# Performance work log

Hardware: AMD Instinct MI355X
Metric: run time of the kernel (lower is better)

Reference implementation:

```python
import jax, jax.numpy as jnp
import numpy as np

HIDDEN = 2048
HEADS = 16
HEAD_DIM = HIDDEN // HEADS  # 128
SCALE = 1.0 / float(np.sqrt(HEAD_DIM))
B, S = 2, 2048


def setup_inputs() -> dict:
    key = jax.random.key(0)
    ks = jax.random.split(key, 5)
    return {
        "x": jax.random.normal(ks[0], (B, S, HIDDEN), dtype=jnp.float32),
        "q_w": jax.random.normal(ks[1], (HIDDEN, HIDDEN), dtype=jnp.float32) * (HIDDEN ** -0.5),
        "k_w": jax.random.normal(ks[2], (HEAD_DIM, HIDDEN), dtype=jnp.float32) * (HIDDEN ** -0.5),
        "v_w": jax.random.normal(ks[3], (HEAD_DIM, HIDDEN), dtype=jnp.float32) * (HIDDEN ** -0.5),
        "o_w": jax.random.normal(ks[4], (HIDDEN, HIDDEN), dtype=jnp.float32) * (HIDDEN ** -0.5),
    }


def reference(x, q_w, k_w, v_w, o_w):
    b, s, _ = x.shape
    # torch F.linear: x @ W^T with W [out, in]
    q = (x @ q_w.T).reshape(b, s, HEADS, HEAD_DIM).transpose(0, 2, 1, 3)  # [B,H,S,D]
    k = x @ k_w.T  # [B,S,D] single shared KV head
    v = x @ v_w.T  # [B,S,D]
    # scores: [B,H,S,S] -- explicit O(S^2) materialization as in the source
    scores = jnp.einsum('bhqd,bkd->bhqk', q, k) * SCALE
    # softmax in float32 then cast back (matches dtype=torch.float32 then type_as)
    attn = jax.nn.softmax(scores.astype(jnp.float32), axis=-1).astype(q.dtype)
    out = jnp.einsum('bhqk,bkd->bhqd', attn, v)  # [B,H,S,D]
    out = out.transpose(0, 2, 1, 3).reshape(b, s, HIDDEN)
    return out @ o_w.T
```

## Files before the change

### kernel.cpp

```cpp
#include <hip/hip_runtime.h>
#include <stdint.h>

#define HID 2048
#define DHEAD 128
#define SEQL 2048
#define C2 0.1275187981510609f
#define MOFF 8.0f

typedef __attribute__((ext_vector_type(4))) float f32x4;
typedef __attribute__((ext_vector_type(8))) short s16x8;

__device__ __forceinline__ unsigned short bf16_rne(float f) {
  union { float f; unsigned u; } v; v.f = f;
  return (unsigned short)((v.u + 0x7FFFu + ((v.u >> 16) & 1u)) >> 16);
}

__device__ __forceinline__ void gload_lds16(const void* g, void* l) {
  __builtin_amdgcn_global_load_lds(
      (__attribute__((address_space(1))) unsigned int*)(void*)g,
      (__attribute__((address_space(3))) unsigned int*)l, 16, 0, 0);
}

__device__ __forceinline__ void cvt8(const float* __restrict__ in,
                                     unsigned short* __restrict__ out, int k) {
  const f32x4* p = (const f32x4*)in;
  f32x4 a = p[2 * k], b = p[2 * k + 1];
  union { s16x8 v; unsigned short s[8]; } o;
  o.s[0] = bf16_rne(a[0]); o.s[1] = bf16_rne(a[1]);
  o.s[2] = bf16_rne(a[2]); o.s[3] = bf16_rne(a[3]);
  o.s[4] = bf16_rne(b[0]); o.s[5] = bf16_rne(b[1]);
  o.s[6] = bf16_rne(b[2]); o.s[7] = bf16_rne(b[3]);
  ((s16x8*)out)[k] = o.v;
}

__global__ __launch_bounds__(256) void cvt_bf16_k(const float* __restrict__ in,
                                                  unsigned short* __restrict__ out,
                                                  int n8) {
  int i = blockIdx.x * 256 + threadIdx.x;
  if (i >= n8) return;
  cvt8(in, out, i);
}

__global__ __launch_bounds__(256) void cvt4_k(
    const float* __restrict__ s0, unsigned short* __restrict__ d0, int n0,
    const float* __restrict__ s1, unsigned short* __restrict__ d1, int n1,
    const float* __restrict__ s2, unsigned short* __restrict__ d2, int n2,
    const float* __restrict__ s3, unsigned short* __restrict__ d3, int n3) {
  int i = blockIdx.x * 256 + threadIdx.x;
  if (i < n0) { cvt8(s0, d0, i); return; }
  i -= n0;
  if (i < n1) { cvt8(s1, d1, i); return; }
  i -= n1;
  if (i < n2) { cvt8(s2, d2, i); return; }
  i -= n2;
  if (i < n3) { cvt8(s3, d3, i); return; }
}

template <int LOG2SLOTS>
__device__ __forceinline__ void stage_tile(const unsigned short* __restrict__ src,
                                           int ld, char* smem, int t) {
  int w = t >> 6;
#pragma unroll
  for (int i = 0; i < 4; ++i) {
    int c = i * 256 + t;
    int row = c >> LOG2SLOTS;
    int slot = c & ((1 << LOG2SLOTS) - 1);
    gload_lds16(src + row * ld + ((slot ^ (row & 7)) << 3),
                smem + (i * 256 + w * 64) * 16);
  }
}

template <int MODE>
__global__ __launch_bounds__(256, 2) void gemm_bt(
    const unsigned short* __restrict__ A, const unsigned short* __restrict__ Bw,
    void* __restrict__ Cout, int M, int N, int K, unsigned short* __restrict__ Vt) {
  __shared__ char As[2][16384];
  __shared__ char Bs[2][16384];
  int t = threadIdx.x;
  int lane = t & 63, w = t >> 6;
  int wm = w >> 1, wn = w & 1;
  int l15 = lane & 15, l4 = lane >> 4;

  int gdx = gridDim.x;
  int nwg = gdx * gridDim.y;
  int bid = blockIdx.y * gdx + blockIdx.x;
  int q8 = nwg >> 3;
  int swz = (bid & 7) * q8 + (bid >> 3);
  int tm = (swz / gdx) * 128, tn = (swz % gdx) * 128;

  f32x4 acc[4][4] = {};

  stage_tile<3>(A + tm * K, K, As[0], t);
  stage_tile<3>(Bw + tn * K, K, Bs[0], t);
  asm volatile("s_waitcnt vmcnt(0)" ::: "memory");
  __builtin_amdgcn_s_barrier();

  int nk = K >> 6;
  for (int ki = 0; ki < nk; ++ki) {
    int cur = ki & 1;
    if (ki + 1 < nk) {
      stage_tile<3>(A + tm * K + (ki + 1) * 64, K, As[cur ^ 1], t);
      stage_tile<3>(Bw + tn * K + (ki + 1) * 64, K, Bs[cur ^ 1], t);
    }
    const char* as = As[cur];
    const char* bs = Bs[cur];
    s16x8 af[4][2], bfr[4][2];
#pragma unroll
    for (int m = 0; m < 4; ++m)
#pragma unroll
      for (int kk = 0; kk < 2; ++kk) {
        int row = wm * 64 + m * 16 + l15;
        af[m][kk] = *(const s16x8*)(as + row * 128 + (((kk * 4 + l4) ^ (row & 7)) << 4));
      }
#pragma unroll
    for (int n = 0; n < 4; ++n)
#pragma unroll
      for (int kk = 0; kk < 2; ++kk) {
        int row = wn * 64 + n * 16 + l15;
        bfr[n][kk] = *(const s16x8*)(bs + row * 128 + (((kk * 4 + l4) ^ (row & 7)) << 4));
      }
#pragma unroll
    for (int m = 0; m < 4; ++m)
#pragma unroll
      for (int n = 0; n < 4; ++n)
#pragma unroll
        for (int kk = 0; kk < 2; ++kk)
          acc[m][n] = __builtin_amdgcn_mfma_f32_16x16x32_bf16(af[m][kk], bfr[n][kk],
                                                              acc[m][n], 0, 0, 0);
    asm volatile("s_waitcnt vmcnt(0) lgkmcnt(0)" ::: "memory");
    __builtin_amdgcn_sched_barrier(0);
    __builtin_amdgcn_s_barrier();
  }

#pragma unroll
  for (int m = 0; m < 4; ++m)
#pragma unroll
    for (int n = 0; n < 4; ++n) {
      int col = tn + wn * 64 + n * 16 + l15;
#pragma unroll
      for (int j = 0; j < 4; ++j) {
        int row = tm + wm * 64 + m * 16 + l4 * 4 + j;
        float v = acc[m][n][j];
        if (MODE == 0) {
          ((unsigned short*)Cout)[row * N + col] = bf16_rne(v);
        } else if (MODE == 1) {
          ((float*)Cout)[row * N + col] = v;
        } else {
          if (col < 128) {
            ((unsigned short*)Cout)[row * 128 + col] = bf16_rne(v);
          } else {
            int d = col - 128, bb = row >> 11, s = row & 2047;
            Vt[((bb * 128 + d) << 11) + s] = bf16_rne(v);
          }
        }
      }
    }
}

__global__ __launch_bounds__(256, 2) void attn_k(
    const unsigned short* __restrict__ Q, const unsigned short* __restrict__ Kb,
    const unsigned short* __restrict__ Vt, unsigned short* __restrict__ AO) {
  __shared__ char Ks[2][16384];
  __shared__ char Vs[2][16384];
  int t = threadIdx.x;
  int lane = t & 63, w = t >> 6;
  int l15 = lane & 15, l4 = lane >> 4;
  int qt = blockIdx.x, bh = blockIdx.y;
  int b = bh >> 4, h = bh & 15;
  int qg = b * SEQL + qt * 128 + w * 32;

  s16x8 qf[2][4];
#pragma unroll
  for (int m = 0; m < 2; ++m)
#pragma unroll
    for (int kc = 0; kc < 4; ++kc)
      qf[m][kc] = *(const s16x8*)(Q + (qg + m * 16 + l15) * HID + h * DHEAD + kc * 32 + l4 * 8);

  union { s16x8 v; unsigned short s[8]; } one_;
#pragma unroll
  for (int i = 0; i < 8; ++i) one_.s[i] = 0x3F80;
  const s16x8 ones = one_.v;

  f32x4 oacc[2][9] = {};

  {
#pragma unroll
    for (int i = 0; i < 4; ++i) {
      int c = i * 256 + t, row = c >> 4, slot = c & 15;
      gload_lds16(Kb + (b * SEQL + row) * DHEAD + ((slot ^ (row & 7)) << 3),
                  Ks[0] + (i * 256 + w * 64) * 16);
    }
#pragma unroll
    for (int i = 0; i < 4; ++i) {
      int c = i * 256 + t, row = c >> 3, slot = c & 7;
      gload_lds16(Vt + (b * DHEAD + row) * SEQL + ((slot ^ (row & 7)) << 3),
                  Vs[0] + (i * 256 + w * 64) * 16);
    }
  }
  asm volatile("s_waitcnt vmcnt(0)" ::: "memory");
  __builtin_amdgcn_s_barrier();

  for (int kv = 0; kv < SEQL; kv += 64) {
    int cur = (kv >> 6) & 1;
    if (kv + 64 < SEQL) {
#pragma unroll
      for (int i = 0; i < 4; ++i) {
        int c = i * 256 + t, row = c >> 4, slot = c & 15;
        gload_lds16(Kb + (b * SEQL + kv + 64 + row) * DHEAD + ((slot ^ (row & 7)) << 3),
                    Ks[cur ^ 1] + (i * 256 + w * 64) * 16);
      }
#pragma unroll
      for (int i = 0; i < 4; ++i) {
        int c = i * 256 + t, row = c >> 3, slot = c & 7;
        gload_lds16(Vt + (b * DHEAD + row) * SEQL + kv + 64 + ((slot ^ (row & 7)) << 3),
                    Vs[cur ^ 1] + (i * 256 + w * 64) * 16);
      }
    }

    const char* ks = Ks[cur];
    const char* vs = Vs[cur];
    char* Psw = Ks[cur] + w * 4096;

    f32x4 sacc[2][4] = {};
#pragma unroll
    for (int n = 0; n < 4; ++n) {
      int krow = n * 16 + l15;
#pragma unroll
      for (int kc = 0; kc < 4; ++kc) {
        s16x8 kf = *(const s16x8*)(ks + krow * 256 + (((kc * 4 + l4) ^ (krow & 7)) << 4));
        sacc[0][n] = __builtin_amdgcn_mfma_f32_16x16x32_bf16(qf[0][kc], kf, sacc[0][n], 0, 0, 0);
        sacc[1][n] = __builtin_amdgcn_mfma_f32_16x16x32_bf16(qf[1][kc], kf, sacc[1][n], 0, 0, 0);
      }
    }

    asm volatile("s_waitcnt lgkmcnt(0)" ::: "memory");
    __builtin_amdgcn_sched_barrier(0);
    __builtin_amdgcn_s_barrier();

#pragma unroll
    for (int m = 0; m < 2; ++m)
#pragma unroll
      for (int n = 0; n < 4; ++n) {
        int pcol = n * 16 + l15;
#pragma unroll
        for (int j = 0; j < 4; ++j) {
          float p = __builtin_amdgcn_exp2f(__builtin_fmaf(sacc[m][n][j], C2, -MOFF));
          int prow = m * 16 + l4 * 4 + j;
          *(unsigned short*)(Psw + prow * 128 + (((pcol >> 3) ^ (prow & 7)) << 4) +
                             (pcol & 7) * 2) = bf16_rne(p);
        }
      }

    asm volatile("s_waitcnt lgkmcnt(0)" ::: "memory");
    __builtin_amdgcn_sched_barrier(0);

#pragma unroll
    for (int kc2 = 0; kc2 < 2; ++kc2) {
      s16x8 pa[2];
#pragma unroll
      for (int m = 0; m < 2; ++m) {
        int row = m * 16 + l15;
        pa[m] = *(const s16x8*)(Psw + row * 128 + (((kc2 * 4 + l4) ^ (row & 7)) << 4));
      }
#pragma unroll
      for (int n = 0; n < 8; ++n) {
        int vrow = n * 16 + l15;
        s16x8 vf = *(const s16x8*)(vs + vrow * 128 + (((kc2 * 4 + l4) ^ (vrow & 7)) << 4));
        oacc[0][n] = __builtin_amdgcn_mfma_f32_16x16x32_bf16(pa[0], vf, oacc[0][n], 0, 0, 0);
        oacc[1][n] = __builtin_amdgcn_mfma_f32_16x16x32_bf16(pa[1], vf, oacc[1][n], 0, 0, 0);
      }
      oacc[0][8] = __builtin_amdgcn_mfma_f32_16x16x32_bf16(pa[0], ones, oacc[0][8], 0, 0, 0);
      oacc[1][8] = __builtin_amdgcn_mfma_f32_16x16x32_bf16(pa[1], ones, oacc[1][8], 0, 0, 0);
    }

    asm volatile("s_waitcnt vmcnt(0) lgkmcnt(0)" ::: "memory");
    __builtin_amdgcn_sched_barrier(0);
    __builtin_amdgcn_s_barrier();
  }

#pragma unroll
  for (int m = 0; m < 2; ++m) {
    float inv[4];
#pragma unroll
    for (int j = 0; j < 4; ++j) inv[j] = 1.f / oacc[m][8][j];
#pragma unroll
    for (int n = 0; n < 8; ++n) {
      int col = h * DHEAD + n * 16 + l15;
#pragma unroll
      for (int j = 0; j < 4; ++j) {
        int row = qg + m * 16 + l4 * 4 + j;
        AO[row * HID + col] = bf16_rne(oacc[m][n][j] * inv[j]);
      }
    }
  }
}

extern "C" void kernel_launch(void* const* d_in, const int* in_sizes, int n_in,
                              void* d_out, int out_size, void* d_ws, size_t ws_size,
                              hipStream_t stream) {
  const float* x  = (const float*)d_in[0];
  const float* qw = (const float*)d_in[1];
  const float* kw = (const float*)d_in[2];
  const float* vw = (const float*)d_in[3];
  const float* ow = (const float*)d_in[4];

  char* ws = (char*)d_ws;
  unsigned short* xb   = (unsigned short*)(ws);
  unsigned short* qwb  = (unsigned short*)(ws + 16777216);
  unsigned short* owb  = qwb;
  unsigned short* kvwb = (unsigned short*)(ws + 25165824);
  unsigned short* Qb   = (unsigned short*)(ws + 26214400);
  unsigned short* Kbuf = (unsigned short*)(ws + 42991616);
  unsigned short* Vtb  = (unsigned short*)(ws + 44040192);
  unsigned short* AOb  = xb;

  cvt4_k<<<6400, 256, 0, stream>>>(x, xb, 1048576, qw, qwb, 524288,
                                   kw, kvwb, 32768, vw, kvwb + 262144, 32768);

  gemm_bt<0><<<dim3(16, 32), 256, 0, stream>>>(xb, qwb, Qb, 4096, 2048, 2048, nullptr);
  cvt_bf16_k<<<2048, 256, 0, stream>>>(ow, owb, 524288);
  gemm_bt<2><<<dim3(2, 32), 256, 0, stream>>>(xb, kvwb, Kbuf, 4096, 256, 2048, Vtb);
  attn_k<<<dim3(16, 32), 256, 0, stream>>>(Qb, Kbuf, Vtb, AOb);
  gemm_bt<1><<<dim3(16, 32), 256, 0, stream>>>(AOb, owb, d_out, 4096, 2048, 2048, nullptr);
}
```

Measured before the change: 219.2 us.

## Fuse K/V projection into Q GEMM and read V directly from global in attention

The Q projection GEMM now covers N=2304 by relying on the K/V weights sitting right after the Q weights in the workspace. Its epilogue routes columns to Q, K or transposed V, which removes the separate small K/V GEMM launch. The attention kernel no longer stages V tiles through LDS. It loads V fragments straight from global memory (through L2) and uses a dedicated per-wave P buffer, which drops one block barrier per KV step. The risk is that the uncached-in-LDS V reads, strided across rows, add global-load latency to the PV MFMA loop.

Measured after the change: 298.9 us. 1.36x slower.

```diff
diff --git a/kernel.cpp b/kernel.cpp
--- a/kernel.cpp
+++ b/kernel.cpp
@@ -73,7 +73,8 @@
 template <int MODE>
 __global__ __launch_bounds__(256, 2) void gemm_bt(
     const unsigned short* __restrict__ A, const unsigned short* __restrict__ Bw,
-    void* __restrict__ Cout, int M, int N, int K, unsigned short* __restrict__ Vt) {
+    void* __restrict__ Cout, int M, int N, int K,
+    unsigned short* __restrict__ Kb, unsigned short* __restrict__ Vt) {
   __shared__ char As[2][16384];
   __shared__ char Bs[2][16384];
   int t = threadIdx.x;
@@ -141,15 +142,15 @@
       for (int j = 0; j < 4; ++j) {
         int row = tm + wm * 64 + m * 16 + l4 * 4 + j;
         float v = acc[m][n][j];
-        if (MODE == 0) {
-          ((unsigned short*)Cout)[row * N + col] = bf16_rne(v);
-        } else if (MODE == 1) {
+        if (MODE == 1) {
           ((float*)Cout)[row * N + col] = v;
         } else {
-          if (col < 128) {
-            ((unsigned short*)Cout)[row * 128 + col] = bf16_rne(v);
+          if (col < 2048) {
+            ((unsigned short*)Cout)[row * 2048 + col] = bf16_rne(v);
+          } else if (col < 2176) {
+            Kb[row * 128 + (col - 2048)] = bf16_rne(v);
           } else {
-            int d = col - 128, bb = row >> 11, s = row & 2047;
+            int d = col - 2176, bb = row >> 11, s = row & 2047;
             Vt[((bb * 128 + d) << 11) + s] = bf16_rne(v);
           }
         }
@@ -161,13 +162,14 @@
     const unsigned short* __restrict__ Q, const unsigned short* __restrict__ Kb,
     const unsigned short* __restrict__ Vt, unsigned short* __restrict__ AO) {
   __shared__ char Ks[2][16384];
-  __shared__ char Vs[2][16384];
+  __shared__ char Ps[4][4096];
   int t = threadIdx.x;
   int lane = t & 63, w = t >> 6;
   int l15 = lane & 15, l4 = lane >> 4;
   int qt = blockIdx.x, bh = blockIdx.y;
   int b = bh >> 4, h = bh & 15;
   int qg = b * SEQL + qt * 128 + w * 32;
+  char* Psw = Ps[w];
 
   s16x8 qf[2][4];
 #pragma unroll
@@ -183,19 +185,11 @@
 
   f32x4 oacc[2][9] = {};
 
-  {
-#pragma unroll
-    for (int i = 0; i < 4; ++i) {
-      int c = i * 256 + t, row = c >> 4, slot = c & 15;
-      gload_lds16(Kb + (b * SEQL + row) * DHEAD + ((slot ^ (row & 7)) << 3),
-                  Ks[0] + (i * 256 + w * 64) * 16);
-    }
-#pragma unroll
-    for (int i = 0; i < 4; ++i) {
-      int c = i * 256 + t, row = c >> 3, slot = c & 7;
-      gload_lds16(Vt + (b * DHEAD + row) * SEQL + ((slot ^ (row & 7)) << 3),
-                  Vs[0] + (i * 256 + w * 64) * 16);
-    }
+#pragma unroll
+  for (int i = 0; i < 4; ++i) {
+    int c = i * 256 + t, row = c >> 4, slot = c & 15;
+    gload_lds16(Kb + (b * SEQL + row) * DHEAD + ((slot ^ (row & 7)) << 3),
+                Ks[0] + (i * 256 + w * 64) * 16);
   }
   asm volatile("s_waitcnt vmcnt(0)" ::: "memory");
   __builtin_amdgcn_s_barrier();
@@ -209,17 +203,9 @@
         gload_lds16(Kb + (b * SEQL + kv + 64 + row) * DHEAD + ((slot ^ (row & 7)) << 3),
                     Ks[cur ^ 1] + (i * 256 + w * 64) * 16);
       }
-#pragma unroll
-      for (int i = 0; i < 4; ++i) {
-        int c = i * 256 + t, row = c >> 3, slot = c & 7;
-        gload_lds16(Vt + (b * DHEAD + row) * SEQL + kv + 64 + ((slot ^ (row & 7)) << 3),
-                    Vs[cur ^ 1] + (i * 256 + w * 64) * 16);
-      }
     }
 
     const char* ks = Ks[cur];
-    const char* vs = Vs[cur];
-    char* Psw = Ks[cur] + w * 4096;
 
     f32x4 sacc[2][4] = {};
 #pragma unroll
@@ -232,10 +218,6 @@
         sacc[1][n] = __builtin_amdgcn_mfma_f32_16x16x32_bf16(qf[1][kc], kf, sacc[1][n], 0, 0, 0);
       }
     }
-
-    asm volatile("s_waitcnt lgkmcnt(0)" ::: "memory");
-    __builtin_amdgcn_sched_barrier(0);
-    __builtin_amdgcn_s_barrier();
 
 #pragma unroll
     for (int m = 0; m < 2; ++m)
@@ -265,7 +247,7 @@
 #pragma unroll
       for (int n = 0; n < 8; ++n) {
         int vrow = n * 16 + l15;
-        s16x8 vf = *(const s16x8*)(vs + vrow * 128 + (((kc2 * 4 + l4) ^ (vrow & 7)) << 4));
+        s16x8 vf = *(const s16x8*)(Vt + (b * DHEAD + vrow) * SEQL + kv + kc2 * 32 + l4 * 8);
         oacc[0][n] = __builtin_amdgcn_mfma_f32_16x16x32_bf16(pa[0], vf, oacc[0][n], 0, 0, 0);
         oacc[1][n] = __builtin_amdgcn_mfma_f32_16x16x32_bf16(pa[1], vf, oacc[1][n], 0, 0, 0);
       }
@@ -317,9 +299,9 @@
   cvt4_k<<<6400, 256, 0, stream>>>(x, xb, 1048576, qw, qwb, 524288,
                                    kw, kvwb, 32768, vw, kvwb + 262144, 32768);
 
-  gemm_bt<0><<<dim3(16, 32), 256, 0, stream>>>(xb, qwb, Qb, 4096, 2048, 2048, nullptr);
+  gemm_bt<0><<<dim3(18, 32), 256, 0, stream>>>(xb, qwb, Qb, 4096, 2304, 2048, Kbuf, Vtb);
   cvt_bf16_k<<<2048, 256, 0, stream>>>(ow, owb, 524288);
-  gemm_bt<2><<<dim3(2, 32), 256, 0, stream>>>(xb, kvwb, Kbuf, 4096, 256, 2048, Vtb);
   attn_k<<<dim3(16, 32), 256, 0, stream>>>(Qb, Kbuf, Vtb, AOb);
-  gemm_bt<1><<<dim3(16, 32), 256, 0, stream>>>(AOb, owb, d_out, 4096, 2048, 2048, nullptr);
-}
+  gemm_bt<1><<<dim3(16, 32), 256, 0, stream>>>(AOb, owb, d_out, 4096, 2048, 2048,
+                                               nullptr, nullptr);
+}
```
